# Performance work log

Measured on AMD Instinct MI355X. Metric: run time of the kernel, lower is better.

Reference implementation:

```python
import jax, jax.numpy as jnp
import numpy as np

B, T, S, H, V = 8, 1024, 1024, 1024, 5000


def setup_inputs() -> dict:
    key = jax.random.key(0)
    ks = jax.random.split(key, 9)
    x = jax.random.normal(ks[0], (B, T, H), dtype=jnp.float32)
    encoder_attn_w = jax.random.uniform(ks[1], (B, T, S), dtype=jnp.float32)
    # normalize like attention weights over source dim
    encoder_attn_w = encoder_attn_w / jnp.sum(encoder_attn_w, axis=-1, keepdims=True)
    nodes = jax.random.randint(ks[2], (B, S), 0, V)
    scale = 0.02
    Wg = jax.random.normal(ks[3], (H, 1), dtype=jnp.float32) * scale
    bg = jnp.zeros((1,), dtype=jnp.float32)
    Wf = jax.random.normal(ks[4], (H, H), dtype=jnp.float32) * scale
    bf = jnp.zeros((H,), dtype=jnp.float32)
    Wv = jax.random.normal(ks[5], (H, V), dtype=jnp.float32) * scale
    bv = jnp.zeros((V,), dtype=jnp.float32)
    return {"x": x, "encoder_attn_w": encoder_attn_w, "nodes": nodes,
            "Wg": Wg, "bg": bg, "Wf": Wf, "bf": bf, "Wv": Wv, "bv": bv}


def reference(x, encoder_attn_w, nodes, Wg, bg, Wf, bf, Wv, bv):
    # Conv1D == affine along last dim (GPT-2 style): x @ W + b
    p_gen = jax.nn.sigmoid(x @ Wg + bg)                      # [B,T,1]
    h = jax.nn.gelu(x @ Wf + bf)                             # fc with activation
    logits = h @ Wv + bv                                     # [B,T,V]
    out = jax.nn.softmax(logits, axis=-1) * p_gen            # gated generate dist
    # pointer/copy: scatter-add attention mass (1 - p_gen) into vocab slots
    add = encoder_attn_w * (1.0 - p_gen)                     # [B,T,S]
    b_idx = jnp.arange(B)[:, None, None]
    t_idx = jnp.arange(T)[None, :, None]
    v_idx = jnp.broadcast_to(nodes[:, None, :], (B, T, S))
    out = out.at[b_idx, t_idx, v_idx].add(add)
    return out
```

## Files before the change

kernel.cpp:

```cpp
#include <hip/hip_runtime.h>

#define Mq   8192
#define Hq   1024
#define Sq   1024
#define Tq   1024
#define Vq   5000
#define Vpad 5120

typedef __bf16 bf16;
typedef bf16  bf16x8 __attribute__((ext_vector_type(8)));
typedef bf16  bf16x4 __attribute__((ext_vector_type(4)));
typedef float f32x4  __attribute__((ext_vector_type(4)));

typedef const __attribute__((address_space(1))) void* gas_t;
typedef __attribute__((address_space(3))) void*       sas_t;

__device__ __forceinline__ void async_copy16(const void* g, void* s) {
  __builtin_amdgcn_global_load_lds((gas_t)g, (sas_t)s, 16, 0, 0);
}

__global__ __launch_bounds__(256) void pgen_cvt(
    const float* __restrict__ x, const float* __restrict__ Wg,
    const float* __restrict__ bg, bf16* __restrict__ xb,
    float* __restrict__ pgen) {
  const int m = blockIdx.x;
  const int t = threadIdx.x;
  float4 v = ((const float4*)(x + (size_t)m * Hq))[t];
  float4 g = ((const float4*)Wg)[t];
  float dot = v.x * g.x + v.y * g.y + v.z * g.z + v.w * g.w;
  bf16x4 o;
  o[0] = (bf16)v.x; o[1] = (bf16)v.y; o[2] = (bf16)v.z; o[3] = (bf16)v.w;
  ((bf16x4*)(xb + (size_t)m * Hq))[t] = o;
  #pragma unroll
  for (int off = 32; off; off >>= 1) dot += __shfl_down(dot, off, 64);
  __shared__ float red[4];
  if ((t & 63) == 0) red[t >> 6] = dot;
  __syncthreads();
  if (t == 0) {
    float s = red[0] + red[1] + red[2] + red[3] + bg[0];
    pgen[m] = 1.0f / (1.0f + __expf(-s));
  }
}

__global__ __launch_bounds__(256) void transpose_cvt(
    const float* __restrict__ W, bf16* __restrict__ WT,
    int K, int Nin, int Npad) {
  __shared__ float tile[32][33];
  const int nb = blockIdx.x * 32, kb = blockIdx.y * 32;
  const int tx = threadIdx.x, ty = threadIdx.y;
  #pragma unroll
  for (int i = 0; i < 32; i += 8) {
    int k = kb + ty + i, n = nb + tx;
    tile[ty + i][tx] = (n < Nin) ? W[(size_t)k * Nin + n] : 0.0f;
  }
  __syncthreads();
  #pragma unroll
  for (int i = 0; i < 32; i += 8) {
    int n = nb + ty + i, k = kb + tx;
    if (n < Npad) WT[(size_t)n * K + k] = (bf16)tile[tx][ty + i];
  }
}

template <int MODE>
__global__ __launch_bounds__(256, 2) void gemm_mfma(
    const bf16* __restrict__ A, const bf16* __restrict__ BT,
    const float* __restrict__ bias, float* __restrict__ outF,
    bf16* __restrict__ outB, int M, int N, int K, int Nstore) {
  __shared__ bf16 As[128 * 32];
  __shared__ bf16 Bs[128 * 32];
  const int tid  = threadIdx.x;
  const int w    = tid >> 6;
  const int l    = tid & 63;
  const int quad = l >> 4;
  const int t16  = l & 15;
  const int wm   = (w >> 1) * 64;
  const int wn   = (w & 1) * 64;
  const int m0   = blockIdx.x * 128;
  const int n0   = blockIdx.y * 128;
  const int srow = l >> 2;
  const int scol = (l & 3) * 8;

  f32x4 acc[4][4] = {};

  for (int k0 = 0; k0 < K; k0 += 32) {
    __syncthreads();
    #pragma unroll
    for (int r = 0; r < 2; ++r) {
      const int chunk = r * 4 + w;
      const int mrow  = chunk * 16 + srow;
      async_copy16(A  + (size_t)(m0 + mrow) * K + k0 + scol, As + chunk * 512);
      async_copy16(BT + (size_t)(n0 + mrow) * K + k0 + scol, Bs + chunk * 512);
    }
    __syncthreads();

    bf16x8 af[4], bfr[4];
    #pragma unroll
    for (int i = 0; i < 4; ++i)
      af[i] = *(const bf16x8*)(As + (wm + 16 * i + t16) * 32 + quad * 8);
    #pragma unroll
    for (int j = 0; j < 4; ++j)
      bfr[j] = *(const bf16x8*)(Bs + (wn + 16 * j + t16) * 32 + quad * 8);
    #pragma unroll
    for (int i = 0; i < 4; ++i)
      #pragma unroll
      for (int j = 0; j < 4; ++j)
        acc[i][j] = __builtin_amdgcn_mfma_f32_16x16x32_bf16(af[i], bfr[j], acc[i][j], 0, 0, 0);
  }

  #pragma unroll
  for (int i = 0; i < 4; ++i) {
    const int mg = m0 + wm + 16 * i + quad * 4;
    #pragma unroll
    for (int j = 0; j < 4; ++j) {
      const int ng = n0 + wn + 16 * j + t16;
      #pragma unroll
      for (int r = 0; r < 4; ++r) {
        float v = acc[i][j][r];
        if (MODE == 0) {
          v += bias[ng];
          float u = 0.7978845608028654f * (v + 0.044715f * v * v * v);
          float gl = 0.5f * v * (1.0f + tanhf(u));
          outB[(size_t)(mg + r) * N + ng] = (bf16)gl;
        } else {
          if (ng < Nstore) {
            v += bias[ng];
            outF[(size_t)(mg + r) * Nstore + ng] = v;
          }
        }
      }
    }
  }
}

__global__ __launch_bounds__(256) void softmax_scatter(
    float* __restrict__ out, const float* __restrict__ pgen,
    const float* __restrict__ attn, const int* __restrict__ nodes) {
  const int m = blockIdx.x;
  const int b = m / Tq;
  float* row = out + (size_t)m * Vq;
  __shared__ float buf[Vq];
  __shared__ float red[4];
  const int t = threadIdx.x;

  float mx = -1e30f;
  float4* buf4 = (float4*)buf;
  const float4* rowLd = (const float4*)row;
  float4* rowSt = (float4*)row;
  for (int i = t; i < Vq / 4; i += 256) {
    float4 v = rowLd[i];
    buf4[i] = v;
    mx = fmaxf(fmaxf(v.x, v.y), fmaxf(fmaxf(v.z, v.w), mx));
  }
  #pragma unroll
  for (int off = 32; off; off >>= 1) mx = fmaxf(mx, __shfl_down(mx, off, 64));
  if ((t & 63) == 0) red[t >> 6] = mx;
  __syncthreads();
  mx = fmaxf(fmaxf(red[0], red[1]), fmaxf(red[2], red[3]));

  float s = 0.0f;
  for (int i = t; i < Vq; i += 256) {
    float e = __expf(buf[i] - mx);
    buf[i] = e;
    s += e;
  }
  #pragma unroll
  for (int off = 32; off; off >>= 1) s += __shfl_down(s, off, 64);
  __syncthreads();
  if ((t & 63) == 0) red[t >> 6] = s;
  __syncthreads();
  s = red[0] + red[1] + red[2] + red[3];

  const float pg = pgen[m];
  const float scale = pg / s;
  for (int i = t; i < Vq; i += 256) buf[i] *= scale;
  __syncthreads();

  const float pc = 1.0f - pg;
  const float* arow = attn + (size_t)m * Sq;
  const int* nrow = nodes + (size_t)b * Sq;
  for (int sIdx = t; sIdx < Sq; sIdx += 256)
    atomicAdd(&buf[nrow[sIdx]], arow[sIdx] * pc);
  __syncthreads();

  for (int i = t; i < Vq / 4; i += 256) {
    rowSt[i] = buf4[i];
  }
}

extern "C" void kernel_launch(void* const* d_in, const int* in_sizes, int n_in,
                              void* d_out, int out_size, void* d_ws, size_t ws_size,
                              hipStream_t stream) {
  const float* x    = (const float*)d_in[0];
  const float* attn = (const float*)d_in[1];
  const int*   nodes= (const int*)d_in[2];
  const float* Wg   = (const float*)d_in[3];
  const float* bg   = (const float*)d_in[4];
  const float* Wf   = (const float*)d_in[5];
  const float* bf_  = (const float*)d_in[6];
  const float* Wv   = (const float*)d_in[7];
  const float* bv   = (const float*)d_in[8];
  float* out = (float*)d_out;

  char* w = (char*)d_ws;
  bf16*  xb   = (bf16*)(w);
  bf16*  h    = (bf16*)(w + 16777216);
  bf16*  WfT  = (bf16*)(w + 33554432);
  bf16*  WvT  = (bf16*)(w + 35651584);
  float* pgen = (float*)(w + 46137344);

  pgen_cvt<<<Mq, 256, 0, stream>>>(x, Wg, bg, xb, pgen);
  transpose_cvt<<<dim3(Hq / 32, Hq / 32), dim3(32, 8), 0, stream>>>(Wf, WfT, Hq, Hq, Hq);
  transpose_cvt<<<dim3(Vpad / 32, Hq / 32), dim3(32, 8), 0, stream>>>(Wv, WvT, Hq, Vq, Vpad);
  gemm_mfma<0><<<dim3(Mq / 128, Hq / 128), 256, 0, stream>>>(
      xb, WfT, bf_, nullptr, h, Mq, Hq, Hq, Hq);
  gemm_mfma<1><<<dim3(Mq / 128, Vpad / 128), 256, 0, stream>>>(
      h, WvT, bv, out, nullptr, Mq, Vpad, Hq, Vq);
  softmax_scatter<<<Mq, 256, 0, stream>>>(out, pgen, attn, nodes);
}
```

Baseline: 458.1 us.

## Fuse exp into logits GEMM epilogue and store bf16 exponentials for finalize

The vocab GEMM epilogue now applies exp to the biased logits directly, with no max subtraction, and writes them as bf16 to workspace when it is large enough, otherwise as fp32 into the output. A new single-pass finalize kernel sums the exponentials, scatter-adds the pre-divided copy mass, and writes the scaled row. This removes the separate max/exp passes and halves the intermediate logits traffic. The bias load is hoisted and tanh in the GELU is replaced by an exp-based form. The risk is overflow for large logits, since nothing is max-stabilised, plus bf16 precision loss on the exponentials.

```diff
diff --git a/kernel.cpp b/kernel.cpp
--- a/kernel.cpp
+++ b/kernel.cpp
@@ -107,6 +107,13 @@
         acc[i][j] = __builtin_amdgcn_mfma_f32_16x16x32_bf16(af[i], bfr[j], acc[i][j], 0, 0, 0);
   }
 
+  float bj[4];
+  #pragma unroll
+  for (int j = 0; j < 4; ++j) {
+    const int ng = n0 + wn + 16 * j + t16;
+    bj[j] = (MODE == 0 || ng < Nstore) ? bias[ng] : 0.0f;
+  }
+
   #pragma unroll
   for (int i = 0; i < 4; ++i) {
     const int mg = m0 + wm + 16 * i + quad * 4;
@@ -115,75 +122,79 @@
       const int ng = n0 + wn + 16 * j + t16;
       #pragma unroll
       for (int r = 0; r < 4; ++r) {
-        float v = acc[i][j][r];
+        float v = acc[i][j][r] + bj[j];
         if (MODE == 0) {
-          v += bias[ng];
-          float u = 0.7978845608028654f * (v + 0.044715f * v * v * v);
-          float gl = 0.5f * v * (1.0f + tanhf(u));
-          outB[(size_t)(mg + r) * N + ng] = (bf16)gl;
+          float u  = 0.7978845608028654f * (v + 0.044715f * v * v * v);
+          float e2 = __expf(2.0f * u);
+          float th = 1.0f - 2.0f / (e2 + 1.0f);
+          outB[(size_t)(mg + r) * N + ng] = (bf16)(0.5f * v * (1.0f + th));
+        } else if (MODE == 1) {
+          if (ng < Nstore)
+            outB[(size_t)(mg + r) * Nstore + ng] = (bf16)__expf(v);
         } else {
-          if (ng < Nstore) {
-            v += bias[ng];
-            outF[(size_t)(mg + r) * Nstore + ng] = v;
-          }
+          if (ng < Nstore)
+            outF[(size_t)(mg + r) * Nstore + ng] = __expf(v);
         }
       }
     }
   }
 }
 
-__global__ __launch_bounds__(256) void softmax_scatter(
-    float* __restrict__ out, const float* __restrict__ pgen,
-    const float* __restrict__ attn, const int* __restrict__ nodes) {
+template <typename ET>
+__global__ __launch_bounds__(256) void finalize(
+    float* __restrict__ out, const ET* __restrict__ e,
+    const float* __restrict__ pgen, const float* __restrict__ attn,
+    const int* __restrict__ nodes) {
   const int m = blockIdx.x;
   const int b = m / Tq;
-  float* row = out + (size_t)m * Vq;
+  const int t = threadIdx.x;
   __shared__ float buf[Vq];
   __shared__ float red[4];
-  const int t = threadIdx.x;
-
-  float mx = -1e30f;
-  float4* buf4 = (float4*)buf;
-  const float4* rowLd = (const float4*)row;
-  float4* rowSt = (float4*)row;
+
+  float s = 0.0f;
+  const ET* erow = e + (size_t)m * Vq;
+  if constexpr (sizeof(ET) == 2) {
+    const bf16x8* e8 = (const bf16x8*)erow;
+    for (int i = t; i < Vq / 8; i += 256) {
+      bf16x8 v = e8[i];
+      #pragma unroll
+      for (int k = 0; k < 8; ++k) {
+        float f = (float)v[k];
+        buf[i * 8 + k] = f;
+        s += f;
+      }
+    }
+  } else {
+    const float4* e4 = (const float4*)erow;
+    for (int i = t; i < Vq / 4; i += 256) {
+      float4 v = e4[i];
+      buf[i * 4 + 0] = v.x; buf[i * 4 + 1] = v.y;
+      buf[i * 4 + 2] = v.z; buf[i * 4 + 3] = v.w;
+      s += (v.x + v.y) + (v.z + v.w);
+    }
+  }
+  #pragma unroll
+  for (int off = 32; off; off >>= 1) s += __shfl_down(s, off, 64);
+  if ((t & 63) == 0) red[t >> 6] = s;
+  __syncthreads();
+  s = red[0] + red[1] + red[2] + red[3];
+
+  const float pg    = pgen[m];
+  const float scale = pg / s;
+  const float coef  = (1.0f - pg) / scale;
+
+  const float* arow = attn + (size_t)m * Sq;
+  const int*   nrow = nodes + (size_t)b * Sq;
+  for (int sIdx = t; sIdx < Sq; sIdx += 256)
+    atomicAdd(&buf[nrow[sIdx]], arow[sIdx] * coef);
+  __syncthreads();
+
+  float4* o4 = (float4*)(out + (size_t)m * Vq);
+  const float4* b4 = (const float4*)buf;
   for (int i = t; i < Vq / 4; i += 256) {
-    float4 v = rowLd[i];
-    buf4[i] = v;
-    mx = fmaxf(fmaxf(v.x, v.y), fmaxf(fmaxf(v.z, v.w), mx));
-  }
-  #pragma unroll
-  for (int off = 32; off; off >>= 1) mx = fmaxf(mx, __shfl_down(mx, off, 64));
-  if ((t & 63) == 0) red[t >> 6] = mx;
-  __syncthreads();
-  mx = fmaxf(fmaxf(red[0], red[1]), fmaxf(red[2], red[3]));
-
-  float s = 0.0f;
-  for (int i = t; i < Vq; i += 256) {
-    float e = __expf(buf[i] - mx);
-    buf[i] = e;
-    s += e;
-  }
-  #pragma unroll
-  for (int off = 32; off; off >>= 1) s += __shfl_down(s, off, 64);
-  __syncthreads();
-  if ((t & 63) == 0) red[t >> 6] = s;
-  __syncthreads();
-  s = red[0] + red[1] + red[2] + red[3];
-
-  const float pg = pgen[m];
-  const float scale = pg / s;
-  for (int i = t; i < Vq; i += 256) buf[i] *= scale;
-  __syncthreads();
-
-  const float pc = 1.0f - pg;
-  const float* arow = attn + (size_t)m * Sq;
-  const int* nrow = nodes + (size_t)b * Sq;
-  for (int sIdx = t; sIdx < Sq; sIdx += 256)
-    atomicAdd(&buf[nrow[sIdx]], arow[sIdx] * pc);
-  __syncthreads();
-
-  for (int i = t; i < Vq / 4; i += 256) {
-    rowSt[i] = buf4[i];
+    float4 v = b4[i];
+    v.x *= scale; v.y *= scale; v.z *= scale; v.w *= scale;
+    o4[i] = v;
   }
 }
 
@@ -202,18 +213,40 @@
   float* out = (float*)d_out;
 
   char* w = (char*)d_ws;
-  bf16*  xb   = (bf16*)(w);
-  bf16*  h    = (bf16*)(w + 16777216);
-  bf16*  WfT  = (bf16*)(w + 33554432);
-  bf16*  WvT  = (bf16*)(w + 35651584);
-  float* pgen = (float*)(w + 46137344);
-
-  pgen_cvt<<<Mq, 256, 0, stream>>>(x, Wg, bg, xb, pgen);
-  transpose_cvt<<<dim3(Hq / 32, Hq / 32), dim3(32, 8), 0, stream>>>(Wf, WfT, Hq, Hq, Hq);
-  transpose_cvt<<<dim3(Vpad / 32, Hq / 32), dim3(32, 8), 0, stream>>>(Wv, WvT, Hq, Vq, Vpad);
-  gemm_mfma<0><<<dim3(Mq / 128, Hq / 128), 256, 0, stream>>>(
-      xb, WfT, bf_, nullptr, h, Mq, Hq, Hq, Hq);
-  gemm_mfma<1><<<dim3(Mq / 128, Vpad / 128), 256, 0, stream>>>(
-      h, WvT, bv, out, nullptr, Mq, Vpad, Hq, Vq);
-  softmax_scatter<<<Mq, 256, 0, stream>>>(out, pgen, attn, nodes);
-}
+
+  const size_t NEED = 111312896ull;
+  const bool big = ws_size >= NEED;
+
+  if (big) {
+    bf16*  eB   = (bf16*)(w);
+    bf16*  xb   = (bf16*)(w);
+    bf16*  hB   = (bf16*)(w + 81920000ull);
+    bf16*  WfT  = (bf16*)(w + 98697216ull);
+    bf16*  WvT  = (bf16*)(w + 100794368ull);
+    float* pgen = (float*)(w + 111280128ull);
+
+    pgen_cvt<<<Mq, 256, 0, stream>>>(x, Wg, bg, xb, pgen);
+    transpose_cvt<<<dim3(Hq / 32, Hq / 32), dim3(32, 8), 0, stream>>>(Wf, WfT, Hq, Hq, Hq);
+    transpose_cvt<<<dim3(Vpad / 32, Hq / 32), dim3(32, 8), 0, stream>>>(Wv, WvT, Hq, Vq, Vpad);
+    gemm_mfma<0><<<dim3(Mq / 128, Hq / 128), 256, 0, stream>>>(
+        xb, WfT, bf_, nullptr, hB, Mq, Hq, Hq, Hq);
+    gemm_mfma<1><<<dim3(Mq / 128, Vpad / 128), 256, 0, stream>>>(
+        hB, WvT, bv, nullptr, eB, Mq, Vpad, Hq, Vq);
+    finalize<bf16><<<Mq, 256, 0, stream>>>(out, eB, pgen, attn, nodes);
+  } else {
+    bf16*  xb   = (bf16*)(w);
+    bf16*  hB   = (bf16*)(w + 16777216);
+    bf16*  WfT  = (bf16*)(w + 33554432);
+    bf16*  WvT  = (bf16*)(w + 35651584);
+    float* pgen = (float*)(w + 46137344);
+
+    pgen_cvt<<<Mq, 256, 0, stream>>>(x, Wg, bg, xb, pgen);
+    transpose_cvt<<<dim3(Hq / 32, Hq / 32), dim3(32, 8), 0, stream>>>(Wf, WfT, Hq, Hq, Hq);
+    transpose_cvt<<<dim3(Vpad / 32, Hq / 32), dim3(32, 8), 0, stream>>>(Wv, WvT, Hq, Vq, Vpad);
+    gemm_mfma<0><<<dim3(Mq / 128, Hq / 128), 256, 0, stream>>>(
+        xb, WfT, bf_, nullptr, hB, Mq, Hq, Hq, Hq);
+    gemm_mfma<2><<<dim3(Mq / 128, Vpad / 128), 256, 0, stream>>>(
+        hB, WvT, bv, out, nullptr, Mq, Vpad, Hq, Vq);
+    finalize<float><<<Mq, 256, 0, stream>>>(out, out, pgen, attn, nodes);
+  }
+}
```

Result: faster. 420.8 us (-8.1%).
